# Performance work log

Measured on AMD Instinct MI355X. Metric: run time of the kernel, lower is better.

## Reference

```python
import jax, jax.numpy as jnp
import numpy as np

N = 8192
IN_F = 256
OUT_F = 64
ALPHA = 0.3  # LeakyReLU negative slope
NEG_INF = -9e15


def setup_inputs() -> dict:
    key = jax.random.key(0)
    k1, k2, k3, k4 = jax.random.split(key, 4)
    h = jax.random.normal(k1, (N, IN_F), dtype=jnp.float32)
    # sparse-ish binary adjacency with self loops (values are 0/1 floats)
    adj = (jax.random.uniform(k2, (N, N)) < 0.05).astype(jnp.float32)
    adj = jnp.maximum(adj, jnp.eye(N, dtype=jnp.float32))
    # xavier_uniform-style scales (gain=1.414)
    w_lim = 1.414 * np.sqrt(6.0 / (IN_F + OUT_F))
    a_lim = 1.414 * np.sqrt(6.0 / (2 * OUT_F + 1))
    W = jax.random.uniform(k3, (IN_F, OUT_F), minval=-w_lim, maxval=w_lim, dtype=jnp.float32)
    a = jax.random.uniform(k4, (2 * OUT_F, 1), minval=-a_lim, maxval=a_lim, dtype=jnp.float32)
    return {"h": h, "adj": adj, "W": W, "a": a}


def reference(h, adj, W, a):
    # Wh: [N, F]
    Wh = h @ W
    # Additive decomposition of the original concat-attention:
    # e_ij = leakyrelu(a[:F].Wh_i + a[F:].Wh_j)  -- identical math, no NxNx2F tensor
    src = Wh @ a[:OUT_F]      # [N, 1]
    dst = Wh @ a[OUT_F:]      # [N, 1]
    e = jax.nn.leaky_relu(src + dst.T, negative_slope=ALPHA)  # [N, N]
    e = e * adj               # faithful: original multiplies by adj before masking
    att = jnp.where(adj > 0, e, NEG_INF)
    att = jax.nn.softmax(att, axis=1)
    # dropout omitted (eval mode / deterministic reference)
    h_prime = att @ Wh        # [N, F]
    return jax.nn.elu(h_prime)
```

## Files before the change

kernel.cpp:

```cpp
#include <hip/hip_runtime.h>
#include <hip/hip_bf16.h>

#define N_NODES 8192
#define IN_F    256
#define OUT_F   64
#define ALPHA   0.3f
#define MBIAS   20.0f
#define CSPL    8
#define COLS_PER (N_NODES / CSPL)
#define NTILES  (COLS_PER / 64)
#define MST     17
#define WH_BLOCKS (N_NODES / 16)

typedef unsigned short u16;
typedef unsigned int   u32;
typedef unsigned long long u64;
typedef __attribute__((ext_vector_type(8))) short bf16x8;
typedef __attribute__((ext_vector_type(4))) float f32x4;

__device__ __forceinline__ float bf2f(u32 u) { return __uint_as_float(u << 16); }
__device__ __forceinline__ u32 f2bfbits(float x) {
    u32 u = __float_as_uint(x);
    return (u + 0x7FFFu + ((u >> 16) & 1u)) >> 16;
}
__device__ __forceinline__ float lrelu(float s) { return s > 0.f ? s : ALPHA * s; }

__device__ __forceinline__ int detect_bf16(const void* adj) {
    return ((((const u32*)adj)[0] & 0xFFFFu) == 0x3F80u) ? 1 : 0;
}

template <bool BF16>
__device__ __forceinline__ float ld(const void* p, size_t idx) {
    if constexpr (BF16) return bf2f(((const u16*)p)[idx]);
    else                return ((const float*)p)[idx];
}

template <bool BF16>
__device__ __forceinline__ void wh4_impl(
    const void* __restrict__ h, const void* __restrict__ W,
    const void* __restrict__ a, float* __restrict__ src,
    float* __restrict__ dst, int i0, int lane, float* accv)
{
    float acc0 = 0.f, acc1 = 0.f, acc2 = 0.f, acc3 = 0.f;
#pragma unroll 8
    for (int k = 0; k < IN_F; ++k) {
        float wv = ld<BF16>(W, (size_t)k * OUT_F + lane);
        float h0 = ld<BF16>(h, (size_t)(i0 + 0) * IN_F + k);
        float h1 = ld<BF16>(h, (size_t)(i0 + 1) * IN_F + k);
        float h2 = ld<BF16>(h, (size_t)(i0 + 2) * IN_F + k);
        float h3 = ld<BF16>(h, (size_t)(i0 + 3) * IN_F + k);
        acc0 = fmaf(h0, wv, acc0);
        acc1 = fmaf(h1, wv, acc1);
        acc2 = fmaf(h2, wv, acc2);
        acc3 = fmaf(h3, wv, acc3);
    }
    float av = ld<BF16>(a, lane);
    float bv = ld<BF16>(a, OUT_F + lane);
    float accs[4] = {acc0, acc1, acc2, acc3};
#pragma unroll
    for (int r = 0; r < 4; ++r) {
        float ps = accs[r] * av, pd = accs[r] * bv;
#pragma unroll
        for (int off = 32; off > 0; off >>= 1) {
            ps += __shfl_xor(ps, off, 64);
            pd += __shfl_xor(pd, off, 64);
        }
        if (lane == 0) { src[i0 + r] = ps; dst[i0 + r] = pd; }
        accv[r] = accs[r];
    }
}

__global__ __launch_bounds__(256) void gat_prep_kernel(
    const void* __restrict__ h, const void* __restrict__ W,
    const void* __restrict__ a, const void* __restrict__ adj,
    u16* __restrict__ WhB, float* __restrict__ src, float* __restrict__ dst,
    u64* __restrict__ mask64)
{
    __shared__ float accs[16][OUT_F];
    const int tid = threadIdx.x, wave = tid >> 6, lane = tid & 63;
    const int isbf = detect_bf16(adj);

    if (blockIdx.x < WH_BLOCKS) {
        const int i0 = blockIdx.x * 16 + wave * 4;
        float av[4];
        if (isbf) wh4_impl<true >(h, W, a, src, dst, i0, lane, av);
        else      wh4_impl<false>(h, W, a, src, dst, i0, lane, av);
#pragma unroll
        for (int r = 0; r < 4; ++r) accs[wave * 4 + r][lane] = av[r];
        __syncthreads();

        const int T = blockIdx.x >> 2, q = blockIdx.x & 3;
        const int nt = wave, n = lane & 15, kg = lane >> 4;
        if ((kg >> 1) == (q & 1)) {
            const int ln0 = (kg & 1) * 8;
            u32 w[4];
#pragma unroll
            for (int e = 0; e < 4; ++e) {
                u32 lo = f2bfbits(accs[ln0 + 2 * e][nt * 16 + n]);
                u32 hi = f2bfbits(accs[ln0 + 2 * e + 1][nt * 16 + n]);
                w[e] = lo | (hi << 16);
            }
            u16* out = WhB + ((size_t)T * 8 + nt * 2 + (q >> 1)) * 512 + lane * 8;
            *(uint4*)out = *(uint4*)w;
        }
    } else {
        const int wgid = (blockIdx.x - WH_BLOCKS) * 4 + wave;
        const int NW   = 2048 * 4;
        const int C    = (N_NODES / 256) * N_NODES;
        if (isbf) {
            const u16* base = (const u16*)adj;
            for (int c = wgid; c < C; c += NW) {
                const u16* p = base + (size_t)c * 256;
                u64 b0 = __ballot(p[lane]       != 0);
                u64 b1 = __ballot(p[64  + lane] != 0);
                u64 b2 = __ballot(p[128 + lane] != 0);
                u64 b3 = __ballot(p[192 + lane] != 0);
                u64 v = (lane == 0) ? b0 : (lane == 1) ? b1 : (lane == 2) ? b2 : b3;
                if (lane < 4) mask64[(size_t)c * 4 + lane] = v;
            }
        } else {
            const float* base = (const float*)adj;
            for (int c = wgid; c < C; c += NW) {
                const float* p = base + (size_t)c * 256;
                u64 b0 = __ballot(p[lane]       != 0.f);
                u64 b1 = __ballot(p[64  + lane] != 0.f);
                u64 b2 = __ballot(p[128 + lane] != 0.f);
                u64 b3 = __ballot(p[192 + lane] != 0.f);
                u64 v = (lane == 0) ? b0 : (lane == 1) ? b1 : (lane == 2) ? b2 : b3;
                if (lane < 4) mask64[(size_t)c * 4 + lane] = v;
            }
        }
    }
}

__global__ __launch_bounds__(256, 4) void gat_attn_kernel(
    const u64* __restrict__ mask64, const u16* __restrict__ WhB,
    const float* __restrict__ src, const float* __restrict__ dst,
    float* __restrict__ O_part, float* __restrict__ l_part)
{
    __shared__ alignas(16) u64  Mlds[64 * MST];
    __shared__ alignas(16) float Dlds[COLS_PER];

    const int tid = threadIdx.x, wave = tid >> 6, lane = tid & 63;
    const int i0 = blockIdx.x * 64, c0 = blockIdx.y * COLS_PER;

    {
        const int r = tid >> 2, q = tid & 3;
        const u64* g = mask64 + (size_t)(i0 + r) * (N_NODES / 64) + (c0 >> 6) + q * 4;
        *(uint4*)&Mlds[r * MST + q * 4]     = *(const uint4*)g;
        *(uint4*)&Mlds[r * MST + q * 4 + 2] = *(const uint4*)(g + 2);
    }
#pragma unroll
    for (int q = 0; q < COLS_PER / 256; ++q)
        Dlds[q * 256 + tid] = dst[c0 + q * 256 + tid];

    __syncthreads();

    const int mrow = lane & 15, kq = (lane >> 4) * 8;
    const int mloc = 16 * wave + mrow;
    const float srow = src[i0 + mloc];
    const float mbound = lrelu(srow + MBIAS);

    const u16* fb = WhB + (size_t)(blockIdx.y * NTILES) * 4096 + lane * 8;

    f32x4 acc[4] = {{0,0,0,0},{0,0,0,0},{0,0,0,0},{0,0,0,0}};
    float lacc = 0.f;

    uint4 bc0 = *(const uint4*)(fb);
    uint4 bc1 = *(const uint4*)(fb + 1024);
    uint4 bc2 = *(const uint4*)(fb + 2048);
    uint4 bc3 = *(const uint4*)(fb + 3072);

    for (int s = 0; s < 2 * NTILES; ++s) {
        const int t = s >> 1, ks = s & 1;

        uint4 bn0, bn1, bn2, bn3;
        if (s + 1 < 2 * NTILES) {
            const int off = ((s + 1) >> 1) * 4096 + ((s + 1) & 1) * 512;
            bn0 = *(const uint4*)(fb + off);
            bn1 = *(const uint4*)(fb + off + 1024);
            bn2 = *(const uint4*)(fb + off + 2048);
            bn3 = *(const uint4*)(fb + off + 3072);
        }

        const u64 mword = Mlds[mloc * MST + t];
        const u32 bits = (u32)(mword >> (ks * 32 + kq)) & 0xFFu;
        const float* dp = &Dlds[t * 64 + ks * 32 + kq];
        float4 dd0 = *(const float4*)dp;
        float4 dd1 = *(const float4*)(dp + 4);
        float dv[8] = {dd0.x,dd0.y,dd0.z,dd0.w, dd1.x,dd1.y,dd1.z,dd1.w};
        union { u32 w[4]; bf16x8 v; } pa;
#pragma unroll
        for (int e = 0; e < 4; ++e) {
            float s0 = lrelu(srow + dv[2 * e]);
            float s1 = lrelu(srow + dv[2 * e + 1]);
            float p0 = (bits & (1u << (2 * e)))     ? __expf(s0 - mbound) : 0.f;
            float p1 = (bits & (1u << (2 * e + 1))) ? __expf(s1 - mbound) : 0.f;
            u32 q0 = f2bfbits(p0), q1 = f2bfbits(p1);
            lacc += bf2f(q0) + bf2f(q1);
            pa.w[e] = q0 | (q1 << 16);
        }

        acc[0] = __builtin_amdgcn_mfma_f32_16x16x32_bf16(pa.v, *(bf16x8*)&bc0, acc[0], 0, 0, 0);
        acc[1] = __builtin_amdgcn_mfma_f32_16x16x32_bf16(pa.v, *(bf16x8*)&bc1, acc[1], 0, 0, 0);
        acc[2] = __builtin_amdgcn_mfma_f32_16x16x32_bf16(pa.v, *(bf16x8*)&bc2, acc[2], 0, 0, 0);
        acc[3] = __builtin_amdgcn_mfma_f32_16x16x32_bf16(pa.v, *(bf16x8*)&bc3, acc[3], 0, 0, 0);

        bc0 = bn0; bc1 = bn1; bc2 = bn2; bc3 = bn3;
    }

    lacc += __shfl_xor(lacc, 16, 64);
    lacc += __shfl_xor(lacc, 32, 64);
    if (lane < 16) l_part[blockIdx.y * N_NODES + i0 + 16 * wave + lane] = lacc;

    float* Ob = O_part + (size_t)blockIdx.y * N_NODES * OUT_F;
#pragma unroll
    for (int nt = 0; nt < 4; ++nt)
#pragma unroll
        for (int reg = 0; reg < 4; ++reg) {
            int row = i0 + 16 * wave + (lane >> 4) * 4 + reg;
            int col = 16 * nt + (lane & 15);
            Ob[(size_t)row * OUT_F + col] = acc[nt][reg];
        }
}

__global__ __launch_bounds__(256) void gat_reduce_kernel(
    const float* __restrict__ O_part, const float* __restrict__ l_part,
    const void* __restrict__ adj, void* __restrict__ out)
{
    int gid = blockIdx.x * 256 + threadIdx.x;
    int i = gid >> 6;
    float O = 0.f, L = 0.f;
#pragma unroll
    for (int c = 0; c < CSPL; ++c) {
        O += O_part[(size_t)c * N_NODES * OUT_F + gid];
        L += l_part[c * N_NODES + i];
    }
    float hp = O / L;
    float o = hp > 0.f ? hp : expm1f(hp);
    if (detect_bf16(adj)) ((u16*)out)[gid] = (u16)f2bfbits(o);
    else                  ((float*)out)[gid] = o;
}

extern "C" void kernel_launch(void* const* d_in, const int* in_sizes, int n_in,
                              void* d_out, int out_size, void* d_ws, size_t ws_size,
                              hipStream_t stream)
{
    const void* h   = d_in[0];
    const void* adj = d_in[1];
    const void* W   = d_in[2];
    const void* a   = d_in[3];

    char* ws = (char*)d_ws;
    u16*   WhB    = (u16*)ws;
    float* src    = (float*)(ws + (1u << 20));
    float* dst    = (float*)(ws + (1u << 20) + 32768);
    u64*   mask64 = (u64*)  (ws + (3u << 20));
    float* O_part = (float*)(ws + (16u << 20));
    float* l_part = (float*)(ws + (32u << 20));

    gat_prep_kernel<<<WH_BLOCKS + 2048, 256, 0, stream>>>(h, W, a, adj, WhB, src, dst, mask64);
    dim3 grid(N_NODES / 64, CSPL);
    gat_attn_kernel<<<grid, 256, 0, stream>>>(mask64, WhB, src, dst, O_part, l_part);
    gat_reduce_kernel<<<N_NODES * OUT_F / 256, 256, 0, stream>>>(O_part, l_part, adj, d_out);
}
```

Measured before the change: 423.4 us.

## Vectorize adjacency mask packing and compute row sums via MFMA with ones

The mask-building phase now loads four adjacency values per lane with one vector load and rearranges the ballot bits into the original column order with bit-spreading arithmetic. In the attention loop, the softmax denominator is accumulated by an extra MFMA against a ones matrix rather than per-lane scalar adds and shuffles. The loop body is also simplified: LeakyReLU via fmaxf, exp computed unconditionally and then selected, and a packed bf16 convert instruction. This trades scalar ALU work for one additional MFMA per step and extra bit-manipulation in mask packing.

Result: slower. 450.6 us (+6.4%).

```diff
diff --git a/kernel.cpp b/kernel.cpp
--- a/kernel.cpp
+++ b/kernel.cpp
@@ -33,6 +33,21 @@
 __device__ __forceinline__ float ld(const void* p, size_t idx) {
     if constexpr (BF16) return bf2f(((const u16*)p)[idx]);
     else                return ((const float*)p)[idx];
+}
+
+__device__ __forceinline__ u64 spread4(u64 x) {
+    x = (x | (x << 24)) & 0x000000FF000000FFull;
+    x = (x | (x << 12)) & 0x000F000F000F000Full;
+    x = (x | (x << 6))  & 0x0303030303030303ull;
+    x = (x | (x << 3))  & 0x1111111111111111ull;
+    return x;
+}
+__device__ __forceinline__ u64 mask_word(u64 b0, u64 b1, u64 b2, u64 b3, int w) {
+    u64 s0 = spread4((b0 >> (16 * w)) & 0xFFFFull);
+    u64 s1 = spread4((b1 >> (16 * w)) & 0xFFFFull);
+    u64 s2 = spread4((b2 >> (16 * w)) & 0xFFFFull);
+    u64 s3 = spread4((b3 >> (16 * w)) & 0xFFFFull);
+    return s0 | (s1 << 1) | (s2 << 2) | (s3 << 3);
 }
 
 template <bool BF16>
@@ -110,24 +125,32 @@
         if (isbf) {
             const u16* base = (const u16*)adj;
             for (int c = wgid; c < C; c += NW) {
-                const u16* p = base + (size_t)c * 256;
-                u64 b0 = __ballot(p[lane]       != 0);
-                u64 b1 = __ballot(p[64  + lane] != 0);
-                u64 b2 = __ballot(p[128 + lane] != 0);
-                u64 b3 = __ballot(p[192 + lane] != 0);
-                u64 v = (lane == 0) ? b0 : (lane == 1) ? b1 : (lane == 2) ? b2 : b3;
-                if (lane < 4) mask64[(size_t)c * 4 + lane] = v;
+                const ushort4 v = *(const ushort4*)(base + (size_t)c * 256 + lane * 4);
+                u64 b0 = __ballot(v.x != 0);
+                u64 b1 = __ballot(v.y != 0);
+                u64 b2 = __ballot(v.z != 0);
+                u64 b3 = __ballot(v.w != 0);
+                u64 o0 = mask_word(b0, b1, b2, b3, 0);
+                u64 o1 = mask_word(b0, b1, b2, b3, 1);
+                u64 o2 = mask_word(b0, b1, b2, b3, 2);
+                u64 o3 = mask_word(b0, b1, b2, b3, 3);
+                u64 vv = (lane == 0) ? o0 : (lane == 1) ? o1 : (lane == 2) ? o2 : o3;
+                if (lane < 4) mask64[(size_t)c * 4 + lane] = vv;
             }
         } else {
             const float* base = (const float*)adj;
             for (int c = wgid; c < C; c += NW) {
-                const float* p = base + (size_t)c * 256;
-                u64 b0 = __ballot(p[lane]       != 0.f);
-                u64 b1 = __ballot(p[64  + lane] != 0.f);
-                u64 b2 = __ballot(p[128 + lane] != 0.f);
-                u64 b3 = __ballot(p[192 + lane] != 0.f);
-                u64 v = (lane == 0) ? b0 : (lane == 1) ? b1 : (lane == 2) ? b2 : b3;
-                if (lane < 4) mask64[(size_t)c * 4 + lane] = v;
+                const float4 v = *(const float4*)(base + (size_t)c * 256 + lane * 4);
+                u64 b0 = __ballot(v.x != 0.f);
+                u64 b1 = __ballot(v.y != 0.f);
+                u64 b2 = __ballot(v.z != 0.f);
+                u64 b3 = __ballot(v.w != 0.f);
+                u64 o0 = mask_word(b0, b1, b2, b3, 0);
+                u64 o1 = mask_word(b0, b1, b2, b3, 1);
+                u64 o2 = mask_word(b0, b1, b2, b3, 2);
+                u64 o3 = mask_word(b0, b1, b2, b3, 3);
+                u64 vv = (lane == 0) ? o0 : (lane == 1) ? o1 : (lane == 2) ? o2 : o3;
+                if (lane < 4) mask64[(size_t)c * 4 + lane] = vv;
             }
         }
     }
@@ -164,7 +187,10 @@
     const u16* fb = WhB + (size_t)(blockIdx.y * NTILES) * 4096 + lane * 8;
 
     f32x4 acc[4] = {{0,0,0,0},{0,0,0,0},{0,0,0,0},{0,0,0,0}};
-    float lacc = 0.f;
+    f32x4 acc_l  = {0, 0, 0, 0};
+    union { u32 w[4]; bf16x8 v; } ones;
+    ones.w[0] = 0x3F803F80u; ones.w[1] = 0x3F803F80u;
+    ones.w[2] = 0x3F803F80u; ones.w[3] = 0x3F803F80u;
 
     uint4 bc0 = *(const uint4*)(fb);
     uint4 bc1 = *(const uint4*)(fb + 1024);
@@ -192,14 +218,20 @@
         union { u32 w[4]; bf16x8 v; } pa;
 #pragma unroll
         for (int e = 0; e < 4; ++e) {
-            float s0 = lrelu(srow + dv[2 * e]);
-            float s1 = lrelu(srow + dv[2 * e + 1]);
-            float p0 = (bits & (1u << (2 * e)))     ? __expf(s0 - mbound) : 0.f;
-            float p1 = (bits & (1u << (2 * e + 1))) ? __expf(s1 - mbound) : 0.f;
-            u32 q0 = f2bfbits(p0), q1 = f2bfbits(p1);
-            lacc += bf2f(q0) + bf2f(q1);
-            pa.w[e] = q0 | (q1 << 16);
-        }
+            float s0 = srow + dv[2 * e];
+            float s1 = srow + dv[2 * e + 1];
+            s0 = fmaxf(s0, ALPHA * s0) - mbound;
+            s1 = fmaxf(s1, ALPHA * s1) - mbound;
+            float p0 = __expf(s0);
+            float p1 = __expf(s1);
+            p0 = (bits & (1u << (2 * e)))     ? p0 : 0.f;
+            p1 = (bits & (1u << (2 * e + 1))) ? p1 : 0.f;
+            u32 pw;
+            asm("v_cvt_pk_bf16_f32 %0, %1, %2" : "=v"(pw) : "v"(p0), "v"(p1));
+            pa.w[e] = pw;
+        }
+
+        acc_l  = __builtin_amdgcn_mfma_f32_16x16x32_bf16(pa.v, ones.v, acc_l, 0, 0, 0);
 
         acc[0] = __builtin_amdgcn_mfma_f32_16x16x32_bf16(pa.v, *(bf16x8*)&bc0, acc[0], 0, 0, 0);
         acc[1] = __builtin_amdgcn_mfma_f32_16x16x32_bf16(pa.v, *(bf16x8*)&bc1, acc[1], 0, 0, 0);
@@ -209,9 +241,11 @@
         bc0 = bn0; bc1 = bn1; bc2 = bn2; bc3 = bn3;
     }
 
-    lacc += __shfl_xor(lacc, 16, 64);
-    lacc += __shfl_xor(lacc, 32, 64);
-    if (lane < 16) l_part[blockIdx.y * N_NODES + i0 + 16 * wave + lane] = lacc;
+    if ((lane & 15) == 0) {
+        float* lp = l_part + (size_t)blockIdx.y * N_NODES + i0 + 16 * wave + (lane >> 4) * 4;
+#pragma unroll
+        for (int reg = 0; reg < 4; ++reg) lp[reg] = acc_l[reg];
+    }
 
     float* Ob = O_part + (size_t)blockIdx.y * N_NODES * OUT_F;
 #pragma unroll
```
